# Kernel optimization log

Measured on AMD Instinct MI355X. Metric: run time of the kernel, lower is better.

The kernel has to match this reference:

```python
import jax, jax.numpy as jnp
import numpy as np

NUM_THRESH = 1000


def setup_inputs() -> dict:
    key = jax.random.key(0)
    k1, k2 = jax.random.split(key)
    B, C, H, W = 16, 4, 512, 512
    inp = jax.random.uniform(k1, (B, C, H, W), dtype=jnp.float32)
    targ = (jax.random.uniform(k2, (B, C, H, W)) < 0.3).astype(jnp.float32)
    return {"input": inp, "target": targ}


def _max_f1_loss(input, target):
    # input, target: [B, C, H, W]; loss = mean_c (1 - max_t F1_c(t))
    B, C, H, W = input.shape
    N = B * H * W
    x = jnp.transpose(input, (1, 0, 2, 3)).reshape(C, N)   # [C, N]
    y = jnp.transpose(target, (1, 0, 2, 3)).reshape(C, N)  # [C, N]
    thresholds = jnp.linspace(0.0, 1.0, NUM_THRESH).astype(jnp.float32)

    def per_class(xc, yc):
        # idx[n] = number of thresholds strictly below xc[n]  (in [0, 1000])
        # sample n is predicted positive (xc > t_k) exactly for k < idx[n]
        idx = jnp.searchsorted(thresholds, xc, side='left')
        s_y = jax.ops.segment_sum(yc, idx, num_segments=NUM_THRESH + 1)
        s_1 = jax.ops.segment_sum(jnp.ones_like(yc), idx, num_segments=NUM_THRESH + 1)
        cum_y = jnp.cumsum(s_y)[:NUM_THRESH]  # sum of y over samples with idx <= k
        cum_1 = jnp.cumsum(s_1)[:NUM_THRESH]
        total_y = jnp.sum(yc)
        TP = total_y - cum_y            # sum(target * pred) per threshold
        PP = jnp.float32(N) - cum_1     # sum(pred) per threshold
        FP = PP - TP                    # sum((1-target) * pred)
        FN = total_y - TP               # sum(target * (1-pred))
        denom = TP + (FN + FP) * 0.5
        F1 = jnp.where(denom == 0, 0.0, TP / jnp.where(denom == 0, 1.0, denom))
        return 1.0 - jnp.max(F1)

    losses = jax.vmap(per_class)(x, y)  # [C]
    return jnp.mean(losses)


def reference(input, target):
    return _max_f1_loss(input, target)
```

## Files before the change

### kernel.cpp

```cpp
#include <hip/hip_runtime.h>

#define NBINS 1001
#define HIST_BLOCK 1024
#define VEC_PER_THREAD 8
#define ELEMS_PER_BLOCK (HIST_BLOCK * VEC_PER_THREAD * 4)

__device__ __forceinline__ int bin_of(float v) {
    double d = ceil((double)v * 999.0);
    int k = (int)d;
    if (k < 0) k = 0;
    if (k > 1000) k = 1000;
    return k;
}

__global__ __launch_bounds__(HIST_BLOCK, 4) void hist_kernel(
    const float* __restrict__ x, const float* __restrict__ y,
    unsigned long long* __restrict__ ghist, int HW, int C)
{
    __shared__ unsigned int lh[NBINS];
    const int tid = threadIdx.x;
    if (tid < NBINS) lh[tid] = 0u;
    __syncthreads();

    const long long start = (long long)blockIdx.x * ELEMS_PER_BLOCK;
    const int c = (int)((start / HW) % C);

    const float4* __restrict__ x4 = (const float4*)(x + start);
    const float4* __restrict__ y4 = (const float4*)(y + start);

    #pragma unroll
    for (int r = 0; r < 2; ++r) {
        float4 xv[4], yv[4];
        #pragma unroll
        for (int k = 0; k < 4; ++k) {
            const int idx = (r * 4 + k) * HIST_BLOCK + tid;
            xv[k] = x4[idx];
            yv[k] = y4[idx];
        }
        #pragma unroll
        for (int k = 0; k < 4; ++k) {
            atomicAdd(&lh[bin_of(xv[k].x)], 1u + ((yv[k].x > 0.5f) ? 0x10000u : 0u));
            atomicAdd(&lh[bin_of(xv[k].y)], 1u + ((yv[k].y > 0.5f) ? 0x10000u : 0u));
            atomicAdd(&lh[bin_of(xv[k].z)], 1u + ((yv[k].z > 0.5f) ? 0x10000u : 0u));
            atomicAdd(&lh[bin_of(xv[k].w)], 1u + ((yv[k].w > 0.5f) ? 0x10000u : 0u));
        }
    }
    __syncthreads();

    if (tid < NBINS) {
        unsigned int v = lh[tid];
        if (v) {
            unsigned long long add = (unsigned long long)(v & 0xffffu)
                                   | ((unsigned long long)(v >> 16) << 32);
            atomicAdd(&ghist[(size_t)c * NBINS + tid], add);
        }
    }
}

__global__ __launch_bounds__(1024) void f1_kernel(
    const unsigned long long* __restrict__ ghist, float* __restrict__ out, int C)
{
    __shared__ unsigned long long wtot[4][16];
    __shared__ float wmax[4][16];
    const int tid  = threadIdx.x;
    const int lane = tid & 63;
    const int wave = tid >> 6;

    unsigned long long v[4];
    #pragma unroll
    for (int c = 0; c < 4; ++c)
        v[c] = (tid < NBINS) ? ghist[(size_t)c * NBINS + tid] : 0ULL;

    #pragma unroll
    for (int off = 1; off < 64; off <<= 1) {
        #pragma unroll
        for (int c = 0; c < 4; ++c) {
            unsigned long long t = __shfl_up(v[c], off, 64);
            if (lane >= off) v[c] += t;
        }
    }
    if (lane == 63) {
        #pragma unroll
        for (int c = 0; c < 4; ++c) wtot[c][wave] = v[c];
    }
    __syncthreads();

    if (wave == 0) {
        const int c = lane >> 4, w = lane & 15;
        unsigned long long t = wtot[c][w];
        #pragma unroll
        for (int off = 1; off < 16; off <<= 1) {
            unsigned long long s = __shfl_up(t, off, 16);
            if (w >= off) t += s;
        }
        wtot[c][w] = t;
    }
    __syncthreads();

    float m[4];
    #pragma unroll
    for (int c = 0; c < 4; ++c) {
        unsigned long long cum = v[c];
        if (wave > 0) cum += wtot[c][wave - 1];
        unsigned long long tot = wtot[c][15];
        unsigned int total_cnt = (unsigned int)(tot & 0xffffffffULL);
        unsigned int total_y   = (unsigned int)(tot >> 32);
        float f1 = 0.0f;
        if (tid < NBINS - 1) {
            unsigned int cnt_cum = (unsigned int)(cum & 0xffffffffULL);
            unsigned int y_cum   = (unsigned int)(cum >> 32);
            unsigned int TP = total_y - y_cum;
            unsigned int PP = total_cnt - cnt_cum;
            unsigned int denom = total_y + PP;
            f1 = (denom == 0u) ? 0.0f : (2.0f * (float)TP) / (float)denom;
        }
        m[c] = f1;
    }

    #pragma unroll
    for (int off = 32; off > 0; off >>= 1) {
        #pragma unroll
        for (int c = 0; c < 4; ++c)
            m[c] = fmaxf(m[c], __shfl_down(m[c], off, 64));
    }
    if (lane == 0) {
        #pragma unroll
        for (int c = 0; c < 4; ++c) wmax[c][wave] = m[c];
    }
    __syncthreads();

    if (tid == 0) {
        float loss = 0.0f;
        #pragma unroll
        for (int c = 0; c < 4; ++c) {
            float mm = wmax[c][0];
            #pragma unroll
            for (int w = 1; w < 16; ++w) mm = fmaxf(mm, wmax[c][w]);
            loss += 1.0f - mm;
        }
        out[0] = loss * 0.25f;
    }
}

extern "C" void kernel_launch(void* const* d_in, const int* in_sizes, int n_in,
                              void* d_out, int out_size, void* d_ws, size_t ws_size,
                              hipStream_t stream) {
    const float* x = (const float*)d_in[0];
    const float* y = (const float*)d_in[1];
    float* out = (float*)d_out;

    const int C = 4, H = 512, W = 512;
    const int HW = H * W;
    const long long total = (long long)in_sizes[0];

    unsigned long long* ghist = (unsigned long long*)d_ws;

    hipMemsetAsync(d_ws, 0, (size_t)C * NBINS * sizeof(unsigned long long), stream);

    const int nblocks = (int)(total / ELEMS_PER_BLOCK);
    hist_kernel<<<nblocks, HIST_BLOCK, 0, stream>>>(x, y, ghist, HW, C);
    f1_kernel<<<1, 1024, 0, stream>>>(ghist, out, C);
    (void)n_in; (void)out_size; (void)ws_size;
}
```

Measured before the change: 151.3 us.

## Split histogram atomics between LDS and 64 replicated global copies

One quarter of the waves in each block now send their histogram updates as 64-bit atomics into one of 64 replicated global histograms instead of shared-memory atomics. The aim is to relieve LDS atomic contention by using L2 atomic throughput in parallel. The F1 kernel then sums the 64 copies per bin before the scan. The memset grows to cover the copies, and the path is only used when the workspace is large enough. Global atomics have higher latency and can contend on hot bins, which may offset the gain.

New measurement: 387.4 us. +156.0%, slower.

```diff
diff --git a/kernel.cpp b/kernel.cpp
--- a/kernel.cpp
+++ b/kernel.cpp
@@ -2,8 +2,9 @@
 
 #define NBINS 1001
 #define HIST_BLOCK 1024
-#define VEC_PER_THREAD 8
-#define ELEMS_PER_BLOCK (HIST_BLOCK * VEC_PER_THREAD * 4)
+#define ELEMS_PER_BLOCK 32768
+#define NCOPIES 64
+#define COPY_STRIDE (4 * NBINS)
 
 __device__ __forceinline__ int bin_of(float v) {
     double d = ceil((double)v * 999.0);
@@ -15,7 +16,9 @@
 
 __global__ __launch_bounds__(HIST_BLOCK, 4) void hist_kernel(
     const float* __restrict__ x, const float* __restrict__ y,
-    unsigned long long* __restrict__ ghist, int HW, int C)
+    unsigned long long* __restrict__ ghist,
+    unsigned long long* __restrict__ gcopies,
+    int HW, int use_split)
 {
     __shared__ unsigned int lh[NBINS];
     const int tid = threadIdx.x;
@@ -23,10 +26,15 @@
     __syncthreads();
 
     const long long start = (long long)blockIdx.x * ELEMS_PER_BLOCK;
-    const int c = (int)((start / HW) % C);
+    const int c = (int)((start / HW) & 3);
 
     const float4* __restrict__ x4 = (const float4*)(x + start);
     const float4* __restrict__ y4 = (const float4*)(y + start);
+
+    const int wave = tid >> 6;
+    const bool go_global = use_split && ((wave & 3) == 3);
+    unsigned long long* gcopy =
+        gcopies + (size_t)(blockIdx.x & (NCOPIES - 1)) * COPY_STRIDE + (size_t)c * NBINS;
 
     #pragma unroll
     for (int r = 0; r < 2; ++r) {
@@ -37,12 +45,22 @@
             xv[k] = x4[idx];
             yv[k] = y4[idx];
         }
-        #pragma unroll
-        for (int k = 0; k < 4; ++k) {
-            atomicAdd(&lh[bin_of(xv[k].x)], 1u + ((yv[k].x > 0.5f) ? 0x10000u : 0u));
-            atomicAdd(&lh[bin_of(xv[k].y)], 1u + ((yv[k].y > 0.5f) ? 0x10000u : 0u));
-            atomicAdd(&lh[bin_of(xv[k].z)], 1u + ((yv[k].z > 0.5f) ? 0x10000u : 0u));
-            atomicAdd(&lh[bin_of(xv[k].w)], 1u + ((yv[k].w > 0.5f) ? 0x10000u : 0u));
+        if (go_global) {
+            #pragma unroll
+            for (int k = 0; k < 4; ++k) {
+                atomicAdd(&gcopy[bin_of(xv[k].x)], 1ULL + ((yv[k].x > 0.5f) ? (1ULL << 32) : 0ULL));
+                atomicAdd(&gcopy[bin_of(xv[k].y)], 1ULL + ((yv[k].y > 0.5f) ? (1ULL << 32) : 0ULL));
+                atomicAdd(&gcopy[bin_of(xv[k].z)], 1ULL + ((yv[k].z > 0.5f) ? (1ULL << 32) : 0ULL));
+                atomicAdd(&gcopy[bin_of(xv[k].w)], 1ULL + ((yv[k].w > 0.5f) ? (1ULL << 32) : 0ULL));
+            }
+        } else {
+            #pragma unroll
+            for (int k = 0; k < 4; ++k) {
+                atomicAdd(&lh[bin_of(xv[k].x)], 1u + ((yv[k].x > 0.5f) ? 0x10000u : 0u));
+                atomicAdd(&lh[bin_of(xv[k].y)], 1u + ((yv[k].y > 0.5f) ? 0x10000u : 0u));
+                atomicAdd(&lh[bin_of(xv[k].z)], 1u + ((yv[k].z > 0.5f) ? 0x10000u : 0u));
+                atomicAdd(&lh[bin_of(xv[k].w)], 1u + ((yv[k].w > 0.5f) ? 0x10000u : 0u));
+            }
         }
     }
     __syncthreads();
@@ -58,7 +76,9 @@
 }
 
 __global__ __launch_bounds__(1024) void f1_kernel(
-    const unsigned long long* __restrict__ ghist, float* __restrict__ out, int C)
+    const unsigned long long* __restrict__ ghist,
+    const unsigned long long* __restrict__ gcopies,
+    float* __restrict__ out, int use_split)
 {
     __shared__ unsigned long long wtot[4][16];
     __shared__ float wmax[4][16];
@@ -70,6 +90,14 @@
     #pragma unroll
     for (int c = 0; c < 4; ++c)
         v[c] = (tid < NBINS) ? ghist[(size_t)c * NBINS + tid] : 0ULL;
+
+    if (use_split && tid < NBINS) {
+        for (int j = 0; j < NCOPIES; ++j) {
+            const unsigned long long* cp = gcopies + (size_t)j * COPY_STRIDE + tid;
+            #pragma unroll
+            for (int c = 0; c < 4; ++c) v[c] += cp[(size_t)c * NBINS];
+        }
+    }
 
     #pragma unroll
     for (int off = 1; off < 64; off <<= 1) {
@@ -149,16 +177,20 @@
     const float* y = (const float*)d_in[1];
     float* out = (float*)d_out;
 
-    const int C = 4, H = 512, W = 512;
+    const int H = 512, W = 512;
     const int HW = H * W;
     const long long total = (long long)in_sizes[0];
 
-    unsigned long long* ghist = (unsigned long long*)d_ws;
+    unsigned long long* ghist   = (unsigned long long*)d_ws;
+    unsigned long long* gcopies = ghist + COPY_STRIDE;
+    const size_t need = (size_t)(1 + NCOPIES) * COPY_STRIDE * sizeof(unsigned long long);
+    const int use_split = (ws_size >= need) ? 1 : 0;
+    const size_t zbytes = use_split ? need : (size_t)COPY_STRIDE * sizeof(unsigned long long);
 
-    hipMemsetAsync(d_ws, 0, (size_t)C * NBINS * sizeof(unsigned long long), stream);
+    hipMemsetAsync(d_ws, 0, zbytes, stream);
 
     const int nblocks = (int)(total / ELEMS_PER_BLOCK);
-    hist_kernel<<<nblocks, HIST_BLOCK, 0, stream>>>(x, y, ghist, HW, C);
-    f1_kernel<<<1, 1024, 0, stream>>>(ghist, out, C);
-    (void)n_in; (void)out_size; (void)ws_size;
+    hist_kernel<<<nblocks, HIST_BLOCK, 0, stream>>>(x, y, ghist, gcopies, HW, use_split);
+    f1_kernel<<<1, 1024, 0, stream>>>(ghist, gcopies, out, use_split);
+    (void)n_in; (void)out_size;
 }
```
